# Kernel tuning notes

Hardware: AMD Instinct MI355X
Metric: run time of the kernel (lower is better)

## Reference

```python
import jax, jax.numpy as jnp
import numpy as np

MIN_LEN = 4      # g.min_word_length
MAX_LEN = 10     # g.max_word_length
THRESH = 0.05    # g.init_threshold
NEG = -1e9


def setup_inputs() -> dict:
    key = jax.random.key(0)
    ks = jax.random.split(key, 6)
    B, L, F, D, U, V = 16, 64, 60, 256, 600, 10000
    x = jax.random.normal(ks[0], (B, L, F), jnp.float32)            # batch dense feat matrix
    unit_feats = jax.random.normal(ks[1], (U, F), jnp.float32)      # per-unit features
    W = jax.random.normal(ks[2], (F, D), jnp.float32) * 0.1         # FeatEmbedding weight
    lengths = jax.random.randint(ks[3], (B,), MIN_LEN, L + 1)       # sentence lengths
    indexed_segments = jax.random.randint(ks[4], (V, MAX_LEN), 0, U)  # vocab -> unit ids
    vocab_length = jax.random.randint(ks[5], (V,), MIN_LEN, MAX_LEN + 1)
    return dict(x=x, unit_feats=unit_feats, W=W, lengths=lengths,
                indexed_segments=indexed_segments, vocab_length=vocab_length)


def reference(x, unit_feats, W, lengths, indexed_segments, vocab_length):
    B, L, _ = x.shape
    V, J = indexed_segments.shape
    # embedding: features -> char_emb space
    word_repr = x @ W                 # [B, L, D]
    unit_repr = unit_feats @ W        # [U, D]
    # cosine similarity between every segment position and every unit
    wn = word_repr / (jnp.linalg.norm(word_repr, axis=-1, keepdims=True) + 1e-8)
    un = unit_repr / (jnp.linalg.norm(unit_repr, axis=-1, keepdims=True) + 1e-8)
    sim = jnp.einsum('bld,ud->blu', wn, un)  # [B, L, U]
    # pad so span gathers past the end read zeros (masked later by `viable`)
    sim_pad = jnp.pad(sim, ((0, 0), (0, J), (0, 0)))
    # accumulate per-position unit scores along each vocab word's unit sequence
    acc = jnp.zeros((B, L, V), sim.dtype)
    per_len = []
    for j in range(J):  # fixed small loop over word-length positions
        # sim at start+j for unit indexed_segments[v, j] -> [B, L, V]
        s_j = sim_pad[:, j:j + L, :][:, :, indexed_segments[:, j]]
        acc = acc + s_j
        if j + 1 >= MIN_LEN:
            per_len.append(acc / (j + 1))  # length-normalized match score
    scores = jnp.stack(per_len, axis=2)  # [B, len_s=L, len_e=E, V]
    E = scores.shape[2]
    k = jnp.arange(E) + MIN_LEN                          # candidate word lengths
    ends = jnp.arange(L)[:, None] + k[None, :] - 1        # [L, E]
    viable = ends[None] < lengths[:, None, None]          # [B, L, E]
    len_match = vocab_length[None, None, None, :] == k[None, None, :, None]
    mask = viable[..., None] & len_match                  # [B, L, E, V]
    masked = jnp.where(mask, scores, NEG)
    # best vocab word per span candidate
    value = masked.max(axis=-1)                           # [B, L, E]
    matched_vocab = masked.argmax(axis=-1)                # [B, L, E]
    matched = value > THRESH
    # best span candidate per batch element (eval path: hard max)
    flat = value.reshape(B, -1)                           # [B, L*E]
    best_inds = flat.argmax(axis=-1)
    best_scores = flat.max(axis=-1)
    best_starts = best_inds // E
    best_ends = best_inds % E + best_starts + MIN_LEN - 1
    any_matched = matched.reshape(B, -1).any(axis=-1)
    best_vocab = jnp.take_along_axis(matched_vocab.reshape(B, -1), best_inds[:, None], axis=1)[:, 0]
    return best_scores, best_starts, best_ends, any_matched, best_vocab
```

## Files before the change

### kernel.cpp

```cpp
#include <hip/hip_runtime.h>
#include <math.h>

#define BB 16
#define LL 64
#define FF 60
#define DD 256
#define UU 600
#define VV 10000
#define JMAX 10
#define MINL 4
#define EE 7
#define NEG (-1e9f)
#define TH 0.05f
#define BCAP 10240

#define UNT_OFF   0
#define WNT_OFF   163840
#define SIM_OFF   425984
#define CNT_OFF   1040384
#define SRT_OFF   1040392
#define VAL_OFF   1613832
#define VOC_OFF   1628168

__global__ __launch_bounds__(256) void k_prep(const int* __restrict__ seg,
                                              const int* __restrict__ vlen,
                                              const float* __restrict__ x,
                                              const float* __restrict__ uf,
                                              const float* __restrict__ W,
                                              unsigned int* __restrict__ cnt,
                                              unsigned int* __restrict__ srt,
                                              float* __restrict__ unT,
                                              float* __restrict__ wnT) {
    int blk = blockIdx.x;
    if (blk < 40) {
        int v = blk * 256 + threadIdx.x;
        if (v >= VV) return;
        int lane = threadIdx.x & 63;
        unsigned long long below = (lane == 0) ? 0ull : (~0ull >> (64 - lane));
        const int* s = seg + v * JMAX;
        unsigned int t[10];
#pragma unroll
        for (int j = 0; j < JMAX; ++j) t[j] = (unsigned int)(s[j] * 11 + j);
        int e = vlen[v] - MINL;
        unsigned int pos = 0;
#pragma unroll
        for (int b2 = 0; b2 < EE; ++b2) {
            unsigned long long m = __ballot(e == b2);
            if (e == b2) {
                int leader = __ffsll((long long)m) - 1;
                unsigned int wc = (unsigned int)__popcll(m);
                unsigned int base = 0;
                if (lane == leader) base = atomicAdd(&cnt[b2], wc);
                base = __shfl(base, leader, 64);
                pos = base + (unsigned int)__popcll(m & below);
            }
        }
        unsigned int* dst = srt + ((size_t)e * BCAP + pos) * 8;
        uint4 qa, qb;
        qa.x = t[0] | (t[1] << 16);
        qa.y = t[2] | (t[3] << 16);
        qa.z = t[4] | (t[5] << 16);
        qa.w = t[6] | (t[7] << 16);
        qb.x = t[8] | (t[9] << 16);
        qb.y = (unsigned int)v;
        qb.z = 0; qb.w = 0;
        ((uint4*)dst)[0] = qa;
        ((uint4*)dst)[1] = qb;
    } else {
        int w = threadIdx.x >> 6;
        int lane = threadIdx.x & 63;
        int id = (blk - 40) * 4 + w;
        const float* row;
        float* outB;
        int stride, col;
        if (id < UU) { row = uf + id * FF; outB = unT; stride = 640;  col = id; }
        else { int bl = id - UU; row = x + bl * FF; outB = wnT; stride = 1024; col = bl; }

        float r0 = 0.f, r1 = 0.f, r2 = 0.f, r3 = 0.f;
#pragma unroll 4
        for (int f = 0; f < FF; ++f) {
            float xv = row[f];
            r0 += xv * W[f * DD + lane];
            r1 += xv * W[f * DD + lane + 64];
            r2 += xv * W[f * DD + lane + 128];
            r3 += xv * W[f * DD + lane + 192];
        }
        float ss = r0 * r0 + r1 * r1 + r2 * r2 + r3 * r3;
#pragma unroll
        for (int m = 32; m > 0; m >>= 1) ss += __shfl_xor(ss, m, 64);
        float inv = 1.0f / (sqrtf(ss) + 1e-8f);
        outB[(lane      ) * stride + col] = r0 * inv;
        outB[(lane +  64) * stride + col] = r1 * inv;
        outB[(lane + 128) * stride + col] = r2 * inv;
        outB[(lane + 192) * stride + col] = r3 * inv;
    }
}

__global__ __launch_bounds__(320) void k_sim(const float* __restrict__ unT,
                                             const float* __restrict__ wnT,
                                             float* __restrict__ sim) {
    int blk = blockIdx.x;
    int b  = blk >> 5;
    int r  = blk & 31;
    int l0 = (r >> 1) * 4;
    int uh = r & 1;
    int bl0 = b * 64 + l0;
    int u = uh * 320 + threadIdx.x;

    float a0 = 0.f, a1 = 0.f, a2 = 0.f, a3 = 0.f;
#pragma unroll 8
    for (int d = 0; d < DD; ++d) {
        float4 wv = *(const float4*)(wnT + d * 1024 + bl0);
        float v  = unT[d * 640 + u];
        a0 += wv.x * v;
        a1 += wv.y * v;
        a2 += wv.z * v;
        a3 += wv.w * v;
    }
    if (u < UU) {
        sim[(bl0 + 0) * UU + u] = a0;
        sim[(bl0 + 1) * UU + u] = a1;
        sim[(bl0 + 2) * UU + u] = a2;
        sim[(bl0 + 3) * UU + u] = a3;
    }
}

template<int K>
__device__ __forceinline__ void seg_pass(const unsigned int* __restrict__ srt,
                                         const float* __restrict__ lds,
                                         int e, int r0, int r1, int lane, int wave,
                                         float (*redS)[8], int (*redV)[8]) {
    float s0 = -1e30f, s1 = -1e30f;
    int w0 = VV, w1 = VV;
    for (int p = r0 + lane; p < r1; p += 64) {
        const uint4* pp = (const uint4*)(srt + ((size_t)e * BCAP + p) * 8);
        uint4 qa = pp[0];
        uint4 qb = pp[1];
        unsigned int tw[5] = {qa.x, qa.y, qa.z, qa.w, qb.x};
        int v = (int)qb.y;
        float a0 = 0.f, a1 = 0.f;
#pragma unroll
        for (int j = 0; j < K; ++j) {
            int idx = (int)((tw[j >> 1] >> ((j & 1) * 16)) & 0xffffu);
            a0 += lds[idx];
            a1 += lds[idx + 1];
        }
        bool p0 = (a0 > s0) || (a0 == s0 && v < w0);
        bool p1 = (a1 > s1) || (a1 == s1 && v < w1);
        s0 = p0 ? a0 : s0;  w0 = p0 ? v : w0;
        s1 = p1 ? a1 : s1;  w1 = p1 ? v : w1;
    }
#pragma unroll
    for (int off = 32; off > 0; off >>= 1) {
        float os0 = __shfl_down(s0, off, 64);
        int   ov0 = __shfl_down(w0, off, 64);
        float os1 = __shfl_down(s1, off, 64);
        int   ov1 = __shfl_down(w1, off, 64);
        if (os0 > s0 || (os0 == s0 && ov0 < w0)) { s0 = os0; w0 = ov0; }
        if (os1 > s1 || (os1 == s1 && ov1 < w1)) { s1 = os1; w1 = ov1; }
    }
    if (lane == 0) {
        redS[e * 2 + 0][wave] = s0; redV[e * 2 + 0][wave] = w0;
        redS[e * 2 + 1][wave] = s1; redV[e * 2 + 1][wave] = w1;
    }
}

__global__ __launch_bounds__(512, 8) void k_score(const float* __restrict__ sim,
                                                  const unsigned int* __restrict__ srt,
                                                  const unsigned int* __restrict__ cnt,
                                                  const int* __restrict__ lengths,
                                                  float* __restrict__ val,
                                                  int* __restrict__ voc) {
    __shared__ float lds[UU * 11];
    __shared__ float redS[14][8];
    __shared__ int   redV[14][8];

    int blk = blockIdx.x;
    int half = blk >> 9;
    int rest = blk & 511;
    int b  = rest >> 5;
    int l0 = (rest & 31) * 2;
    int tid = threadIdx.x;

    if (tid < 112) {
        redS[tid >> 3][tid & 7] = -1e30f;
        redV[tid >> 3][tid & 7] = VV;
    }
    for (int u = tid; u < UU; u += 512) {
#pragma unroll
        for (int r = 0; r < 11; ++r) {
            int m = l0 + r;
            lds[u * 11 + r] = (m < LL) ? sim[(b * 64 + m) * UU + u] : 0.0f;
        }
    }
    __syncthreads();

    int wave = tid >> 6, lane = tid & 63;

    unsigned nlo[EE], nhi[EE], Bw[EE];
    unsigned Wtot = 0;
#pragma unroll
    for (int e = 0; e < EE; ++e) {
        unsigned n = cnt[e];
        unsigned lo = half ? (n >> 1) : 0;
        unsigned hi = half ? n : (n >> 1);
        nlo[e] = lo; nhi[e] = hi;
        Bw[e] = Wtot;
        Wtot += (hi - lo) * (unsigned)(e + MINL);
    }
    unsigned qlo = (unsigned)(((unsigned long long)Wtot * (unsigned)wave) >> 3);
    unsigned qhi = (unsigned)(((unsigned long long)Wtot * (unsigned)(wave + 1)) >> 3);

#pragma unroll
    for (int e = 0; e < EE; ++e) {
        unsigned K = (unsigned)(e + MINL);
        unsigned segw = (nhi[e] - nlo[e]) * K;
        unsigned Be = Bw[e];
        if (qhi <= Be || qlo >= Be + segw || segw == 0) continue;
        unsigned a = (qlo > Be) ? (qlo - Be) : 0;
        unsigned bb = qhi - Be; if (bb > segw) bb = segw;
        int r0 = (int)(nlo[e] + (a + K - 1) / K);
        int r1 = (int)(nlo[e] + (bb + K - 1) / K);
        if (r1 <= r0) continue;
        switch (e) {
            case 0: seg_pass<4> (srt, lds, 0, r0, r1, lane, wave, redS, redV); break;
            case 1: seg_pass<5> (srt, lds, 1, r0, r1, lane, wave, redS, redV); break;
            case 2: seg_pass<6> (srt, lds, 2, r0, r1, lane, wave, redS, redV); break;
            case 3: seg_pass<7> (srt, lds, 3, r0, r1, lane, wave, redS, redV); break;
            case 4: seg_pass<8> (srt, lds, 4, r0, r1, lane, wave, redS, redV); break;
            case 5: seg_pass<9> (srt, lds, 5, r0, r1, lane, wave, redS, redV); break;
            case 6: seg_pass<10>(srt, lds, 6, r0, r1, lane, wave, redS, redV); break;
        }
    }
    __syncthreads();

    if (tid < 14) {
        int e  = tid >> 1;
        int dl = tid & 1;
        float s = redS[tid][0];
        int  vv = redV[tid][0];
#pragma unroll
        for (int w2 = 1; w2 < 8; ++w2) {
            float os = redS[tid][w2];
            int   ov = redV[tid][w2];
            if (os > s || (os == s && ov < vv)) { s = os; vv = ov; }
        }
        int lg = l0 + dl;
        int k = e + MINL;
        bool viable = (lg + k - 1) < lengths[b];
        float sn = s / (float)k;
        int o = (half * BB * LL + b * 64 + lg) * EE + e;
        val[o] = viable ? sn : NEG;
        voc[o] = viable ? vv : 0;
    }
}

__global__ __launch_bounds__(512) void k_final(const float* __restrict__ val,
                                               const int* __restrict__ voc,
                                               float* __restrict__ out) {
    __shared__ float sS[8];
    __shared__ int   sI[8];
    __shared__ int   sV[8];
    __shared__ int   sA[8];
    int b = blockIdx.x;
    int t = threadIdx.x;
    float s = -3e38f;
    int idx = 1 << 30;
    int vc = 0;
    int any = 0;
    if (t < LL * EE) {
        int o0 = b * LL * EE + t;
        int o1 = BB * LL * EE + o0;
        float s0 = val[o0], s1 = val[o1];
        int   v0 = voc[o0], v1 = voc[o1];
        bool sel = (s1 > s0) || (s1 == s0 && v1 < v0);
        s  = sel ? s1 : s0;
        vc = sel ? v1 : v0;
        idx = t;
        any = (s > TH) ? 1 : 0;
    }
#pragma unroll
    for (int off = 32; off > 0; off >>= 1) {
        float os = __shfl_down(s, off, 64);
        int   oi = __shfl_down(idx, off, 64);
        int   ov = __shfl_down(vc, off, 64);
        int   oa = __shfl_down(any, off, 64);
        if (os > s || (os == s && oi < idx)) { s = os; idx = oi; vc = ov; }
        any |= oa;
    }
    int w = t >> 6, lane = t & 63;
    if (lane == 0) { sS[w] = s; sI[w] = idx; sV[w] = vc; sA[w] = any; }
    __syncthreads();
    if (t == 0) {
        for (int w2 = 1; w2 < 8; ++w2) {
            float os = sS[w2];
            int   oi = sI[w2];
            if (os > s || (os == s && oi < idx)) { s = os; idx = oi; vc = sV[w2]; }
            any |= sA[w2];
        }
        int start = idx / EE;
        int e = idx - start * EE;
        int end = e + start + MINL - 1;
        out[b]      = s;
        out[16 + b] = (float)start;
        out[32 + b] = (float)end;
        out[48 + b] = any ? 1.0f : 0.0f;
        out[64 + b] = (float)vc;
    }
}

extern "C" void kernel_launch(void* const* d_in, const int* in_sizes, int n_in,
                              void* d_out, int out_size, void* d_ws, size_t ws_size,
                              hipStream_t stream) {
    const float* x       = (const float*)d_in[0];
    const float* uf      = (const float*)d_in[1];
    const float* W       = (const float*)d_in[2];
    const int*   lengths = (const int*)d_in[3];
    const int*   seg     = (const int*)d_in[4];
    const int*   vlen    = (const int*)d_in[5];
    float* out = (float*)d_out;
    float* ws  = (float*)d_ws;

    float*        unT = ws + UNT_OFF;
    float*        wnT = ws + WNT_OFF;
    float*        sim = ws + SIM_OFF;
    unsigned int* cnt = (unsigned int*)(ws + CNT_OFF);
    unsigned int* srt = (unsigned int*)(ws + SRT_OFF);
    float*        val = ws + VAL_OFF;
    int*          voc = (int*)(ws + VOC_OFF);

    hipMemsetAsync(cnt, 0, 8 * sizeof(unsigned int), stream);
    k_prep<<<446, 256, 0, stream>>>(seg, vlen, x, uf, W, cnt, srt, unT, wnT);
    k_sim<<<512, 320, 0, stream>>>(unT, wnT, sim);
    k_score<<<1024, 512, 0, stream>>>(sim, srt, cnt, lengths, val, voc);
    k_final<<<BB, 512, 0, stream>>>(val, voc, out);
}
```

Before: 132.8 us.

## Score four start positions per block and skip non-viable spans and rows

k_score now has each block handle four consecutive start positions instead of two. Every vocab entry's packed unit indices therefore feed four accumulators, which halves the block count and the re-reading of the sorted vocab per position. Blocks whose start positions all lie past the sentence length write NEG and exit early, and length groups that cannot fit are removed from the per-wave work split. k_sim also skips row tiles beyond each sentence's length. The LDS tile grows to 13 rows and registers per thread increase, which may lower occupancy. Sim rows left unwritten may still be read as padding for non-viable spans.

```diff
diff --git a/kernel.cpp b/kernel.cpp
--- a/kernel.cpp
+++ b/kernel.cpp
@@ -40,7 +40,7 @@
         const int* s = seg + v * JMAX;
         unsigned int t[10];
 #pragma unroll
-        for (int j = 0; j < JMAX; ++j) t[j] = (unsigned int)(s[j] * 11 + j);
+        for (int j = 0; j < JMAX; ++j) t[j] = (unsigned int)(s[j] * 13 + j);
         int e = vlen[v] - MINL;
         unsigned int pos = 0;
 #pragma unroll
@@ -98,11 +98,13 @@
 
 __global__ __launch_bounds__(320) void k_sim(const float* __restrict__ unT,
                                              const float* __restrict__ wnT,
+                                             const int* __restrict__ lengths,
                                              float* __restrict__ sim) {
     int blk = blockIdx.x;
     int b  = blk >> 5;
     int r  = blk & 31;
     int l0 = (r >> 1) * 4;
+    if (l0 >= lengths[b]) return;
     int uh = r & 1;
     int bl0 = b * 64 + l0;
     int u = uh * 320 + threadIdx.x;
@@ -126,42 +128,53 @@
 }
 
 template<int K>
-__device__ __forceinline__ void seg_pass(const unsigned int* __restrict__ srt,
-                                         const float* __restrict__ lds,
-                                         int e, int r0, int r1, int lane, int wave,
-                                         float (*redS)[8], int (*redV)[8]) {
-    float s0 = -1e30f, s1 = -1e30f;
-    int w0 = VV, w1 = VV;
+__device__ __forceinline__ void seg_pass4(const unsigned int* __restrict__ srt,
+                                          const float* __restrict__ lds,
+                                          int e, int r0, int r1, int lane, int wave,
+                                          float (*redS)[8], int (*redV)[8]) {
+    float s0 = -1e30f, s1 = -1e30f, s2 = -1e30f, s3 = -1e30f;
+    int w0 = VV, w1 = VV, w2 = VV, w3 = VV;
     for (int p = r0 + lane; p < r1; p += 64) {
         const uint4* pp = (const uint4*)(srt + ((size_t)e * BCAP + p) * 8);
         uint4 qa = pp[0];
         uint4 qb = pp[1];
         unsigned int tw[5] = {qa.x, qa.y, qa.z, qa.w, qb.x};
         int v = (int)qb.y;
-        float a0 = 0.f, a1 = 0.f;
+        float a0 = 0.f, a1 = 0.f, a2 = 0.f, a3 = 0.f;
 #pragma unroll
         for (int j = 0; j < K; ++j) {
             int idx = (int)((tw[j >> 1] >> ((j & 1) * 16)) & 0xffffu);
             a0 += lds[idx];
             a1 += lds[idx + 1];
+            a2 += lds[idx + 2];
+            a3 += lds[idx + 3];
         }
         bool p0 = (a0 > s0) || (a0 == s0 && v < w0);
         bool p1 = (a1 > s1) || (a1 == s1 && v < w1);
+        bool p2 = (a2 > s2) || (a2 == s2 && v < w2);
+        bool p3 = (a3 > s3) || (a3 == s3 && v < w3);
         s0 = p0 ? a0 : s0;  w0 = p0 ? v : w0;
         s1 = p1 ? a1 : s1;  w1 = p1 ? v : w1;
+        s2 = p2 ? a2 : s2;  w2 = p2 ? v : w2;
+        s3 = p3 ? a3 : s3;  w3 = p3 ? v : w3;
     }
 #pragma unroll
     for (int off = 32; off > 0; off >>= 1) {
-        float os0 = __shfl_down(s0, off, 64);
-        int   ov0 = __shfl_down(w0, off, 64);
-        float os1 = __shfl_down(s1, off, 64);
-        int   ov1 = __shfl_down(w1, off, 64);
-        if (os0 > s0 || (os0 == s0 && ov0 < w0)) { s0 = os0; w0 = ov0; }
-        if (os1 > s1 || (os1 == s1 && ov1 < w1)) { s1 = os1; w1 = ov1; }
+        float os; int ov;
+        os = __shfl_down(s0, off, 64); ov = __shfl_down(w0, off, 64);
+        if (os > s0 || (os == s0 && ov < w0)) { s0 = os; w0 = ov; }
+        os = __shfl_down(s1, off, 64); ov = __shfl_down(w1, off, 64);
+        if (os > s1 || (os == s1 && ov < w1)) { s1 = os; w1 = ov; }
+        os = __shfl_down(s2, off, 64); ov = __shfl_down(w2, off, 64);
+        if (os > s2 || (os == s2 && ov < w2)) { s2 = os; w2 = ov; }
+        os = __shfl_down(s3, off, 64); ov = __shfl_down(w3, off, 64);
+        if (os > s3 || (os == s3 && ov < w3)) { s3 = os; w3 = ov; }
     }
     if (lane == 0) {
-        redS[e * 2 + 0][wave] = s0; redV[e * 2 + 0][wave] = w0;
-        redS[e * 2 + 1][wave] = s1; redV[e * 2 + 1][wave] = w1;
+        redS[e * 4 + 0][wave] = s0; redV[e * 4 + 0][wave] = w0;
+        redS[e * 4 + 1][wave] = s1; redV[e * 4 + 1][wave] = w1;
+        redS[e * 4 + 2][wave] = s2; redV[e * 4 + 2][wave] = w2;
+        redS[e * 4 + 3][wave] = s3; redV[e * 4 + 3][wave] = w3;
     }
 }
 
@@ -171,26 +184,38 @@
                                                   const int* __restrict__ lengths,
                                                   float* __restrict__ val,
                                                   int* __restrict__ voc) {
-    __shared__ float lds[UU * 11];
-    __shared__ float redS[14][8];
-    __shared__ int   redV[14][8];
+    __shared__ float lds[UU * 13];
+    __shared__ float redS[28][8];
+    __shared__ int   redV[28][8];
 
     int blk = blockIdx.x;
-    int half = blk >> 9;
-    int rest = blk & 511;
-    int b  = rest >> 5;
-    int l0 = (rest & 31) * 2;
+    int half = blk >> 8;
+    int rest = blk & 255;
+    int b  = rest >> 4;
+    int l0 = (rest & 15) * 4;
     int tid = threadIdx.x;
-
-    if (tid < 112) {
+    int len = lengths[b];
+
+    if (l0 + MINL - 1 >= len) {
+        if (tid < 28) {
+            int e  = tid >> 2;
+            int dl = tid & 3;
+            int o = (half * BB * LL + b * 64 + l0 + dl) * EE + e;
+            val[o] = NEG;
+            voc[o] = 0;
+        }
+        return;
+    }
+
+    if (tid < 224) {
         redS[tid >> 3][tid & 7] = -1e30f;
         redV[tid >> 3][tid & 7] = VV;
     }
     for (int u = tid; u < UU; u += 512) {
 #pragma unroll
-        for (int r = 0; r < 11; ++r) {
+        for (int r = 0; r < 13; ++r) {
             int m = l0 + r;
-            lds[u * 11 + r] = (m < LL) ? sim[(b * 64 + m) * UU + u] : 0.0f;
+            lds[u * 13 + r] = (m < LL) ? sim[(b * 64 + m) * UU + u] : 0.0f;
         }
     }
     __syncthreads();
@@ -204,6 +229,7 @@
         unsigned n = cnt[e];
         unsigned lo = half ? (n >> 1) : 0;
         unsigned hi = half ? n : (n >> 1);
+        if (l0 + e + MINL - 1 >= len) { lo = 0; hi = 0; }
         nlo[e] = lo; nhi[e] = hi;
         Bw[e] = Wtot;
         Wtot += (hi - lo) * (unsigned)(e + MINL);
@@ -223,20 +249,20 @@
         int r1 = (int)(nlo[e] + (bb + K - 1) / K);
         if (r1 <= r0) continue;
         switch (e) {
-            case 0: seg_pass<4> (srt, lds, 0, r0, r1, lane, wave, redS, redV); break;
-            case 1: seg_pass<5> (srt, lds, 1, r0, r1, lane, wave, redS, redV); break;
-            case 2: seg_pass<6> (srt, lds, 2, r0, r1, lane, wave, redS, redV); break;
-            case 3: seg_pass<7> (srt, lds, 3, r0, r1, lane, wave, redS, redV); break;
-            case 4: seg_pass<8> (srt, lds, 4, r0, r1, lane, wave, redS, redV); break;
-            case 5: seg_pass<9> (srt, lds, 5, r0, r1, lane, wave, redS, redV); break;
-            case 6: seg_pass<10>(srt, lds, 6, r0, r1, lane, wave, redS, redV); break;
+            case 0: seg_pass4<4> (srt, lds, 0, r0, r1, lane, wave, redS, redV); break;
+            case 1: seg_pass4<5> (srt, lds, 1, r0, r1, lane, wave, redS, redV); break;
+            case 2: seg_pass4<6> (srt, lds, 2, r0, r1, lane, wave, redS, redV); break;
+            case 3: seg_pass4<7> (srt, lds, 3, r0, r1, lane, wave, redS, redV); break;
+            case 4: seg_pass4<8> (srt, lds, 4, r0, r1, lane, wave, redS, redV); break;
+            case 5: seg_pass4<9> (srt, lds, 5, r0, r1, lane, wave, redS, redV); break;
+            case 6: seg_pass4<10>(srt, lds, 6, r0, r1, lane, wave, redS, redV); break;
         }
     }
     __syncthreads();
 
-    if (tid < 14) {
-        int e  = tid >> 1;
-        int dl = tid & 1;
+    if (tid < 28) {
+        int e  = tid >> 2;
+        int dl = tid & 3;
         float s = redS[tid][0];
         int  vv = redV[tid][0];
 #pragma unroll
@@ -247,7 +273,7 @@
         }
         int lg = l0 + dl;
         int k = e + MINL;
-        bool viable = (lg + k - 1) < lengths[b];
+        bool viable = (lg + k - 1) < len;
         float sn = s / (float)k;
         int o = (half * BB * LL + b * 64 + lg) * EE + e;
         val[o] = viable ? sn : NEG;
@@ -331,7 +357,7 @@
 
     hipMemsetAsync(cnt, 0, 8 * sizeof(unsigned int), stream);
     k_prep<<<446, 256, 0, stream>>>(seg, vlen, x, uf, W, cnt, srt, unT, wnT);
-    k_sim<<<512, 320, 0, stream>>>(unT, wnT, sim);
-    k_score<<<1024, 512, 0, stream>>>(sim, srt, cnt, lengths, val, voc);
+    k_sim<<<512, 320, 0, stream>>>(unT, wnT, lengths, sim);
+    k_score<<<512, 512, 0, stream>>>(sim, srt, cnt, lengths, val, voc);
     k_final<<<BB, 512, 0, stream>>>(val, voc, out);
 }
```

New measurement: 131.4 us. Within noise of the previous version (-1.1%).
